# Kernel optimization log

Hardware: AMD Instinct MI355X
Metric: run time of the kernel (lower is better)

The kernel has to match this reference:

```python
import jax, jax.numpy as jnp
import numpy as np

D_MODEL = 512
NHEAD = 8
NUM_LAYERS = 2
INPUT_DIM = 16
DELTA_SCALE = 1.5
LN_EPS = 1e-5


def setup_inputs() -> dict:
    key = jax.random.key(0)
    ks = jax.random.split(key, 16)
    B, S = 16, 1024
    D = D_MODEL
    s_in = 1.0 / np.sqrt(INPUT_DIM)
    s_d = 1.0 / np.sqrt(D)
    return {
        "features": jax.random.normal(ks[0], (B, S, INPUT_DIM), dtype=jnp.float32),
        "hist_w": jax.random.uniform(ks[1], (D, INPUT_DIM), jnp.float32, -s_in, s_in),
        "hist_b": jax.random.uniform(ks[2], (D,), jnp.float32, -s_in, s_in),
        "query_w": jax.random.uniform(ks[3], (D, INPUT_DIM), jnp.float32, -s_in, s_in),
        "query_b": jax.random.uniform(ks[4], (D,), jnp.float32, -s_in, s_in),
        "in_proj_w": jax.random.uniform(ks[5], (NUM_LAYERS, 3 * D, D), jnp.float32, -s_d, s_d),
        "in_proj_b": jnp.zeros((NUM_LAYERS, 3 * D), jnp.float32),
        "attn_out_w": jax.random.uniform(ks[6], (NUM_LAYERS, D, D), jnp.float32, -s_d, s_d),
        "attn_out_b": jnp.zeros((NUM_LAYERS, D), jnp.float32),
        "ln_g": jnp.ones((NUM_LAYERS, D), jnp.float32),
        "ln_b": jnp.zeros((NUM_LAYERS, D), jnp.float32),
        "out_proj_w": jax.random.uniform(ks[7], (1, D), jnp.float32, -s_d, s_d),
        "out_proj_b": jax.random.uniform(ks[8], (1,), jnp.float32, -s_d, s_d),
    }


def _layer_norm(x, g, b):
    mu = jnp.mean(x, axis=-1, keepdims=True)
    var = jnp.var(x, axis=-1, keepdims=True)
    return (x - mu) * jax.lax.rsqrt(var + LN_EPS) * g + b


def _causal_mha(x, kv, wi, bi, wo, bo):
    # x: [B,S,D] queries, kv: [B,S,D] keys/values; query t attends to kv[:t+1]
    B, S, D = x.shape
    hd = D // NHEAD
    wq, wk, wv = wi[:D], wi[D:2 * D], wi[2 * D:]
    bq, bk, bv = bi[:D], bi[D:2 * D], bi[2 * D:]
    q = (x @ wq.T + bq).reshape(B, S, NHEAD, hd)
    k = (kv @ wk.T + bk).reshape(B, S, NHEAD, hd)
    v = (kv @ wv.T + bv).reshape(B, S, NHEAD, hd)
    scale = 1.0 / np.sqrt(hd)
    scores = jnp.einsum('bqhd,bkhd->bhqk', q, k) * scale
    causal = jnp.tril(jnp.ones((S, S), dtype=bool))
    scores = jnp.where(causal, scores, jnp.finfo(scores.dtype).min)
    attn = jax.nn.softmax(scores, axis=-1)
    out = jnp.einsum('bhqk,bkhd->bqhd', attn, v).reshape(B, S, D)
    return out @ wo.T + bo


def reference(features, hist_w, hist_b, query_w, query_b, in_proj_w, in_proj_b,
              attn_out_w, attn_out_b, ln_g, ln_b, out_proj_w, out_proj_b):
    history = features @ hist_w.T + hist_b          # [B,S,D] (fixed K/V)
    x = features @ query_w.T + query_b              # [B,S,D] queries
    for l in range(NUM_LAYERS):
        a = _causal_mha(x, history, in_proj_w[l], in_proj_b[l], attn_out_w[l], attn_out_b[l])
        x = _layer_norm(x + a, ln_g[l], ln_b[l])
    raw = (x @ out_proj_w.T + out_proj_b)[..., 0]   # [B,S]
    return DELTA_SCALE * jnp.tanh(raw)
```

## Files before the change

### kernel.cpp

```cpp
#include <hip/hip_runtime.h>
#include <math.h>

#define DM 512
#define NH 8
#define HD 64
#define BB 16
#define SS 1024
#define NROWS (BB*SS)
#define IND 16
#define KD 512

typedef unsigned short u16;
typedef __attribute__((ext_vector_type(8))) short bf16x8;
typedef __attribute__((ext_vector_type(4))) float f32x4;

static __device__ __forceinline__ u16 f2bf(float f) {
  union { float f; unsigned int u; } v; v.f = f;
  unsigned int r = v.u + 0x7FFFu + ((v.u >> 16) & 1u);
  return (u16)(r >> 16);
}

static __device__ __forceinline__ float dot4(float4 a, float4 b) {
  return a.x*b.x + a.y*b.y + a.z*b.z + a.w*b.w;
}

__global__ __launch_bounds__(256) void k_f2bf_v(const float* __restrict__ in,
                                                u16* __restrict__ out, int n4) {
  int i = blockIdx.x * 256 + threadIdx.x;
  if (i < n4) {
    float4 v = ((const float4*)in)[i];
    ushort4 p;
    p.x = f2bf(v.x); p.y = f2bf(v.y); p.z = f2bf(v.z); p.w = f2bf(v.w);
    ((ushort4*)out)[i] = p;
  }
}

__global__ __launch_bounds__(256) void k_input_proj(
    const float* __restrict__ feat, const float* __restrict__ hw, const float* __restrict__ hb,
    const float* __restrict__ qw, const float* __restrict__ qb,
    u16* __restrict__ histb, float* __restrict__ x, u16* __restrict__ xb) {
  int r0 = blockIdx.x * 16;
  int tid = threadIdx.x;
  int w = tid >> 6, lane = tid & 63;
  __shared__ float f[16][16];
  f[tid >> 4][tid & 15] = feat[(size_t)(r0 + (tid >> 4))*IND + (tid & 15)];
  __syncthreads();

  #pragma unroll
  for (int ch = 0; ch < 2; ch++) {
    int c0 = ch*256 + lane*4;
    {
      float4 wv[4][4];
      #pragma unroll
      for (int j=0;j<4;j++)
        #pragma unroll
        for (int kq=0;kq<4;kq++)
          wv[j][kq] = *(const float4*)(hw + (size_t)(c0+j)*IND + kq*4);
      float b0 = hb[c0], b1 = hb[c0+1], b2 = hb[c0+2], b3 = hb[c0+3];
      #pragma unroll
      for (int rr=0; rr<4; rr++) {
        int row = r0 + w*4 + rr;
        const float4* fr = (const float4*)f[w*4 + rr];
        float4 f0 = fr[0], f1 = fr[1], f2 = fr[2], f3 = fr[3];
        float v0 = b0 + dot4(wv[0][0],f0) + dot4(wv[0][1],f1) + dot4(wv[0][2],f2) + dot4(wv[0][3],f3);
        float v1 = b1 + dot4(wv[1][0],f0) + dot4(wv[1][1],f1) + dot4(wv[1][2],f2) + dot4(wv[1][3],f3);
        float v2 = b2 + dot4(wv[2][0],f0) + dot4(wv[2][1],f1) + dot4(wv[2][2],f2) + dot4(wv[2][3],f3);
        float v3 = b3 + dot4(wv[3][0],f0) + dot4(wv[3][1],f1) + dot4(wv[3][2],f2) + dot4(wv[3][3],f3);
        ushort4 hp; hp.x = f2bf(v0); hp.y = f2bf(v1); hp.z = f2bf(v2); hp.w = f2bf(v3);
        *(ushort4*)&histb[(size_t)row*DM + c0] = hp;
      }
    }
    {
      float4 wv[4][4];
      #pragma unroll
      for (int j=0;j<4;j++)
        #pragma unroll
        for (int kq=0;kq<4;kq++)
          wv[j][kq] = *(const float4*)(qw + (size_t)(c0+j)*IND + kq*4);
      float b0 = qb[c0], b1 = qb[c0+1], b2 = qb[c0+2], b3 = qb[c0+3];
      #pragma unroll
      for (int rr=0; rr<4; rr++) {
        int row = r0 + w*4 + rr;
        const float4* fr = (const float4*)f[w*4 + rr];
        float4 f0 = fr[0], f1 = fr[1], f2 = fr[2], f3 = fr[3];
        float v0 = b0 + dot4(wv[0][0],f0) + dot4(wv[0][1],f1) + dot4(wv[0][2],f2) + dot4(wv[0][3],f3);
        float v1 = b1 + dot4(wv[1][0],f0) + dot4(wv[1][1],f1) + dot4(wv[1][2],f2) + dot4(wv[1][3],f3);
        float v2 = b2 + dot4(wv[2][0],f0) + dot4(wv[2][1],f1) + dot4(wv[2][2],f2) + dot4(wv[2][3],f3);
        float v3 = b3 + dot4(wv[3][0],f0) + dot4(wv[3][1],f1) + dot4(wv[3][2],f2) + dot4(wv[3][3],f3);
        float4 xv; xv.x = v0; xv.y = v1; xv.z = v2; xv.w = v3;
        *(float4*)&x[(size_t)row*DM + c0] = xv;
        ushort4 xp; xp.x = f2bf(v0); xp.y = f2bf(v1); xp.z = f2bf(v2); xp.w = f2bf(v3);
        *(ushort4*)&xb[(size_t)row*DM + c0] = xp;
      }
    }
  }
}

template<int EPI>
__global__ __launch_bounds__(256) void k_bgemm(
    const u16* __restrict__ A, const u16* __restrict__ Wb,
    const float* __restrict__ bias,
    float* __restrict__ Cf, u16* __restrict__ C0h, u16* __restrict__ C1h) {
  __shared__ u16 As[128*64];
  __shared__ u16 Bs[128*64];
  int bm = blockIdx.y * 128, bn = blockIdx.x * 128;
  int tid = threadIdx.x;
  int w = tid >> 6, lane = tid & 63;
  int wm = (w >> 1) * 64, wn = (w & 1) * 64;
  int lq = lane & 15, g = lane >> 4, l7 = lq & 7;

  int srow = tid >> 1;
  int su0 = (tid & 1) * 4;
  const u16* Ag = A  + (size_t)(bm + srow)*KD + su0*8;
  const u16* Bg = Wb + (size_t)(bn + srow)*KD + su0*8;
  int sw[4];
  #pragma unroll
  for (int i=0;i<4;i++) sw[i] = srow*64 + (((su0+i) ^ (srow&7)) << 3);

  f32x4 acc[4][4];
  #pragma unroll
  for (int mf=0;mf<4;mf++)
    #pragma unroll
    for (int nf=0;nf<4;nf++) acc[mf][nf] = (f32x4){0.f,0.f,0.f,0.f};

  #pragma unroll 1
  for (int k0 = 0; k0 < KD; k0 += 64) {
    bf16x8 ar[4], br[4];
    #pragma unroll
    for (int i=0;i<4;i++) {
      ar[i] = *(const bf16x8*)(Ag + k0 + i*8);
      br[i] = *(const bf16x8*)(Bg + k0 + i*8);
    }
    __syncthreads();
    #pragma unroll
    for (int i=0;i<4;i++) { *(bf16x8*)&As[sw[i]] = ar[i]; *(bf16x8*)&Bs[sw[i]] = br[i]; }
    __syncthreads();
    #pragma unroll
    for (int ks=0; ks<2; ks++) {
      int un = ((g + 4*ks) ^ l7) << 3;
      bf16x8 af[4], bfr[4];
      #pragma unroll
      for (int mf=0;mf<4;mf++) af[mf]  = *(const bf16x8*)&As[(wm + mf*16 + lq)*64 + un];
      #pragma unroll
      for (int nf=0;nf<4;nf++) bfr[nf] = *(const bf16x8*)&Bs[(wn + nf*16 + lq)*64 + un];
      #pragma unroll
      for (int mf=0;mf<4;mf++)
        #pragma unroll
        for (int nf=0;nf<4;nf++)
          acc[mf][nf] = __builtin_amdgcn_mfma_f32_16x16x32_bf16(af[mf], bfr[nf], acc[mf][nf], 0, 0, 0);
    }
  }

  float fb[4];
  #pragma unroll
  for (int nf=0;nf<4;nf++) fb[nf] = bias[bn + wn + nf*16 + lq];
  int m0 = bm + wm + g*4;
  int n0 = bn + wn + lq;

  if (EPI == 1 || (EPI == 2 && bn < 512)) {
    const float sc = (EPI == 1) ? 0.125f : 1.0f;
    #pragma unroll
    for (int mf=0;mf<4;mf++) {
      int mb = m0 + mf*16;
      int b = mb >> 10, s = mb & 1023;
      #pragma unroll
      for (int nf=0;nf<4;nf++) {
        int n = n0 + nf*16;
        int h = (n >> 6) & 7, d = n & 63;
        u16* dst = C0h + (((size_t)(b*NH + h))*SS + s)*HD + d;
        #pragma unroll
        for (int r=0;r<4;r++) dst[r*HD] = f2bf((acc[mf][nf][r] + fb[nf]) * sc);
      }
    }
  } else if (EPI == 2) {
    #pragma unroll
    for (int mf=0;mf<4;mf++) {
      int mb = m0 + mf*16;
      int b = mb >> 10, s = mb & 1023;
      #pragma unroll
      for (int nf=0;nf<4;nf++) {
        int n = n0 + nf*16 - 512;
        int h = n >> 6, d = n & 63;
        ushort4 pk;
        pk.x = f2bf(acc[mf][nf][0] + fb[nf]);
        pk.y = f2bf(acc[mf][nf][1] + fb[nf]);
        pk.z = f2bf(acc[mf][nf][2] + fb[nf]);
        pk.w = f2bf(acc[mf][nf][3] + fb[nf]);
        *(ushort4*)&C1h[(((size_t)(b*NH + h))*HD + d)*SS + s] = pk;
      }
    }
  } else {
    #pragma unroll
    for (int mf=0;mf<4;mf++) {
      #pragma unroll
      for (int r=0;r<4;r++) {
        int m = m0 + mf*16 + r;
        #pragma unroll
        for (int nf=0;nf<4;nf++) {
          int n = n0 + nf*16;
          Cf[(size_t)m*DM + n] = acc[mf][nf][r] + fb[nf] + Cf[(size_t)m*DM + n];
        }
      }
    }
  }
}

__global__ __launch_bounds__(512) void k_attn_mfma(
    const u16* __restrict__ Q, const u16* __restrict__ K,
    const u16* __restrict__ Vt, u16* __restrict__ ctxb) {
  int ip = blockIdx.x;
  int bh = blockIdx.y;
  int b = bh >> 3, h = bh & 7;
  int tid = threadIdx.x;
  int w = tid >> 6, lane = tid & 63;
  int lq = lane & 15, g = lane >> 4;
  int l7 = lq & 7;

  __shared__ u16 Ks[4096];
  __shared__ u16 Vs[4096];
  __shared__ u16 Ps[8192];

  int sr = tid >> 3, su = tid & 7;
  int kw = sr*64 + ((su ^ (sr&7)) << 3);
  const u16* kgb = K + ((size_t)bh*SS + sr)*HD + su*8;
  const u16* vgb = Vt + ((size_t)bh*HD + sr)*SS + su*8;
  int pbase = w*1024;

  bf16x8 kreg = *(const bf16x8*)kgb;
  bf16x8 vreg = *(const bf16x8*)vgb;

  #pragma unroll 1
  for (int half = 0; half < 2; half++) {
    int qt2 = half ? (7 - ip) : ip;
    int last = 2*qt2 + 1;

    const u16* qbase = Q + ((size_t)bh*SS + qt2*128 + w*16 + lq)*HD;
    bf16x8 qa0 = *(const bf16x8*)(qbase + g*8);
    bf16x8 qa1 = *(const bf16x8*)(qbase + g*8 + 32);

    f32x4 o[4];
    #pragma unroll
    for (int nb=0;nb<4;nb++) o[nb] = (f32x4){0.f,0.f,0.f,0.f};
    float mrun[4], lrun[4];
    #pragma unroll
    for (int r=0;r<4;r++) { mrun[r] = -1e30f; lrun[r] = 0.f; }

    #pragma unroll 1
    for (int kt = 0; kt <= last; kt++) {
      __syncthreads();
      *(bf16x8*)&Ks[kw] = kreg;
      *(bf16x8*)&Vs[kw] = vreg;
      __syncthreads();
      if (kt < last) {
        kreg = *(const bf16x8*)(kgb + (size_t)(kt+1)*64*HD);
        vreg = *(const bf16x8*)(vgb + (kt+1)*64);
      } else if (half == 0) {
        kreg = *(const bf16x8*)kgb;
        vreg = *(const bf16x8*)vgb;
      }
      if (kt*64 > qt2*128 + w*16 + 15) continue;

      f32x4 s[4];
      #pragma unroll
      for (int nb=0;nb<4;nb++) s[nb] = (f32x4){0.f,0.f,0.f,0.f};
      #pragma unroll
      for (int ks=0; ks<2; ks++) {
        bf16x8 aq = ks ? qa1 : qa0;
        #pragma unroll
        for (int nb=0;nb<4;nb++) {
          bf16x8 kb = *(const bf16x8*)&Ks[(lq + 16*nb)*64 + (((g + 4*ks) ^ l7) << 3)];
          s[nb] = __builtin_amdgcn_mfma_f32_16x16x32_bf16(aq, kb, s[nb], 0, 0, 0);
        }
      }

      bool diag = (kt*64 + 63 > qt2*128 + w*16);
      #pragma unroll
      for (int r=0;r<4;r++) {
        int qrow = qt2*128 + w*16 + g*4 + r;
        if (diag) {
          #pragma unroll
          for (int nb=0;nb<4;nb++)
            if (kt*64 + lq + 16*nb > qrow) s[nb][r] = -1e30f;
        }
        float rm = fmaxf(fmaxf(s[0][r], s[1][r]), fmaxf(s[2][r], s[3][r]));
        #pragma unroll
        for (int off=1; off<16; off<<=1) rm = fmaxf(rm, __shfl_xor(rm, off));
        float mnew = fmaxf(mrun[r], rm);
        float corr = __expf(mrun[r] - mnew);
        float psum = 0.f;
        int mrow = g*4 + r;
        #pragma unroll
        for (int nb=0;nb<4;nb++) {
          float p = __expf(s[nb][r] - mnew);
          psum += p;
          Ps[pbase + mrow*64 + ((((lq>>3) + 2*nb) ^ (mrow&7)) << 3) + l7] = f2bf(p);
        }
        #pragma unroll
        for (int off=1; off<16; off<<=1) psum += __shfl_xor(psum, off);
        lrun[r] = lrun[r]*corr + psum;
        mrun[r] = mnew;
        #pragma unroll
        for (int nb=0;nb<4;nb++) o[nb][r] *= corr;
      }

      #pragma unroll
      for (int ks=0; ks<2; ks++) {
        bf16x8 pa = *(const bf16x8*)&Ps[pbase + lq*64 + (((g + 4*ks) ^ l7) << 3)];
        #pragma unroll
        for (int nb=0;nb<4;nb++) {
          bf16x8 vb = *(const bf16x8*)&Vs[(lq + 16*nb)*64 + (((g + 4*ks) ^ l7) << 3)];
          o[nb] = __builtin_amdgcn_mfma_f32_16x16x32_bf16(pa, vb, o[nb], 0, 0, 0);
        }
      }
    }

    #pragma unroll
    for (int r=0;r<4;r++) {
      float inv = 1.f / lrun[r];
      int qrow = qt2*128 + w*16 + g*4 + r;
      u16* cp = ctxb + ((size_t)b*SS + qrow)*DM + h*HD;
      #pragma unroll
      for (int nb=0;nb<4;nb++) cp[lq + 16*nb] = f2bf(o[nb][r] * inv);
    }
  }
}

__global__ __launch_bounds__(256) void k_ln(
    float* __restrict__ x, const float* __restrict__ g,
    const float* __restrict__ b, u16* __restrict__ xb) {
  int row = blockIdx.x*4 + (threadIdx.x>>6);
  int lane = threadIdx.x & 63;
  float* xr = x + (size_t)row*DM;
  float vals[8]; float s1=0.f, s2=0.f;
  #pragma unroll
  for (int u=0;u<8;u++){ float vv = xr[lane + 64*u]; vals[u]=vv; s1+=vv; s2+=vv*vv; }
  #pragma unroll
  for (int off=1; off<64; off<<=1){ s1 += __shfl_xor(s1,off); s2 += __shfl_xor(s2,off); }
  float mu  = s1 * (1.0f/DM);
  float var = s2 * (1.0f/DM) - mu*mu;
  float inv = rsqrtf(var + 1e-5f);
  u16* xbr = xb + (size_t)row*DM;
  #pragma unroll
  for (int u=0;u<8;u++){
    int c = lane+64*u;
    float vv = (vals[u]-mu)*inv*g[c] + b[c];
    xr[c] = vv;
    xbr[c] = f2bf(vv);
  }
}

__global__ __launch_bounds__(256) void k_head(
    const float* __restrict__ x, const float* __restrict__ w,
    const float* __restrict__ b, float* __restrict__ out) {
  int row = blockIdx.x*4 + (threadIdx.x>>6);
  int lane = threadIdx.x & 63;
  const float* xr = x + (size_t)row*DM;
  float acc = 0.f;
  #pragma unroll
  for (int u=0;u<8;u++) acc += xr[lane+64*u]*w[lane+64*u];
  #pragma unroll
  for (int off=1; off<64; off<<=1) acc += __shfl_xor(acc,off);
  if (lane == 0) out[row] = 1.5f * tanhf(acc + b[0]);
}

extern "C" void kernel_launch(void* const* d_in, const int* in_sizes, int n_in,
                              void* d_out, int out_size, void* d_ws, size_t ws_size,
                              hipStream_t stream) {
  (void)in_sizes; (void)n_in; (void)out_size; (void)ws_size;
  const float* feat      = (const float*)d_in[0];
  const float* hist_w    = (const float*)d_in[1];
  const float* hist_b    = (const float*)d_in[2];
  const float* query_w   = (const float*)d_in[3];
  const float* query_b   = (const float*)d_in[4];
  const float* in_proj_w = (const float*)d_in[5];
  const float* in_proj_b = (const float*)d_in[6];
  const float* attn_w    = (const float*)d_in[7];
  const float* attn_b    = (const float*)d_in[8];
  const float* ln_g      = (const float*)d_in[9];
  const float* ln_b      = (const float*)d_in[10];
  const float* out_w     = (const float*)d_in[11];
  const float* out_b     = (const float*)d_in[12];
  float* out = (float*)d_out;

  float* ws = (float*)d_ws;
  const size_t P = (size_t)NROWS * DM;
  float* x    = ws;
  u16* xb     = (u16*)(ws + P);
  u16* histb  = xb + P;
  u16* ctxb   = histb + P;
  u16* qbf    = ctxb + P;
  u16* kbf    = qbf + P;
  u16* vtb    = kbf + P;
  u16* wipb   = vtb + P;
  u16* wob    = wipb + (size_t)2*3*DM*DM;

  {
    int n4i = 2*3*DM*DM/4, n4o = 2*DM*DM/4;
    k_f2bf_v<<<(n4i+255)/256, 256, 0, stream>>>(in_proj_w, wipb, n4i);
    k_f2bf_v<<<(n4o+255)/256, 256, 0, stream>>>(attn_w, wob, n4o);
  }
  k_input_proj<<<NROWS/16, 256, 0, stream>>>(feat, hist_w, hist_b, query_w, query_b, histb, x, xb);

  for (int l = 0; l < 2; l++) {
    const u16* wq  = wipb + (size_t)l*3*DM*DM;
    const u16* wkv = wq + (size_t)DM*DM;
    const float* bq  = in_proj_b + (size_t)l*3*DM;
    const float* bkv = bq + DM;
    k_bgemm<1><<<dim3(4, 128), 256, 0, stream>>>(xb,    wq,  bq,  nullptr, qbf, nullptr);
    k_bgemm<2><<<dim3(8, 128), 256, 0, stream>>>(histb, wkv, bkv, nullptr, kbf, vtb);
    dim3 ga(4, BB*NH);
    k_attn_mfma<<<ga, 512, 0, stream>>>(qbf, kbf, vtb, ctxb);
    const u16* wo = wob + (size_t)l*DM*DM;
    const float* bo = attn_b + (size_t)l*DM;
    k_bgemm<3><<<dim3(4, 128), 256, 0, stream>>>(ctxb, wo, bo, x, nullptr, nullptr);
    k_ln<<<NROWS/4, 256, 0, stream>>>(x, ln_g + (size_t)l*DM, ln_b + (size_t)l*DM, xb);
  }
  k_head<<<NROWS/4, 256, 0, stream>>>(x, out_w, out_b, out);
}
```

Measured before the change: 422.0 us.

## Double-buffer GEMM tiles with direct global-to-LDS loads

The bf16 GEMM now stages A and B tiles straight from global memory into shared memory using global_load_lds, skipping the register round trip. The shared buffers are doubled so the next K tile is fetched while MFMAs run on the current one, and there is one barrier per iteration instead of two. The XOR swizzle moves into the per-lane global addresses so the LDS layout still matches the fragment reads. This doubles LDS use to 64 KB per block, which may reduce occupancy, and correctness depends on how the builtin orders and waits on its asynchronous writes to LDS.

```diff
diff --git a/kernel.cpp b/kernel.cpp
--- a/kernel.cpp
+++ b/kernel.cpp
@@ -23,6 +23,11 @@
 static __device__ __forceinline__ float dot4(float4 a, float4 b) {
   return a.x*b.x + a.y*b.y + a.z*b.z + a.w*b.w;
 }
+
+#define GLOAD_LDS16(gp, lp)                                                  \
+  __builtin_amdgcn_global_load_lds(                                          \
+      (const __attribute__((address_space(1))) void*)(gp),                   \
+      (__attribute__((address_space(3))) void*)(lp), 16, 0, 0)
 
 __global__ __launch_bounds__(256) void k_f2bf_v(const float* __restrict__ in,
                                                 u16* __restrict__ out, int n4) {
@@ -101,21 +106,18 @@
     const u16* __restrict__ A, const u16* __restrict__ Wb,
     const float* __restrict__ bias,
     float* __restrict__ Cf, u16* __restrict__ C0h, u16* __restrict__ C1h) {
-  __shared__ u16 As[128*64];
-  __shared__ u16 Bs[128*64];
+  __shared__ u16 As[2][128*64];
+  __shared__ u16 Bs[2][128*64];
   int bm = blockIdx.y * 128, bn = blockIdx.x * 128;
   int tid = threadIdx.x;
-  int w = tid >> 6, lane = tid & 63;
-  int wm = (w >> 1) * 64, wn = (w & 1) * 64;
+  int wv = tid >> 6, lane = tid & 63;
+  int wm = (wv >> 1) * 64, wn = (wv & 1) * 64;
   int lq = lane & 15, g = lane >> 4, l7 = lq & 7;
 
-  int srow = tid >> 1;
-  int su0 = (tid & 1) * 4;
-  const u16* Ag = A  + (size_t)(bm + srow)*KD + su0*8;
-  const u16* Bg = Wb + (size_t)(bn + srow)*KD + su0*8;
-  int sw[4];
-  #pragma unroll
-  for (int i=0;i<4;i++) sw[i] = srow*64 + (((su0+i) ^ (srow&7)) << 3);
+  int rsub = lane >> 3;
+  int sug  = (lane & 7) ^ rsub;
+  const u16* Ag = A  + (size_t)(bm + wv*32 + rsub)*KD + sug*8;
+  const u16* Bg = Wb + (size_t)(bn + wv*32 + rsub)*KD + sug*8;
 
   f32x4 acc[4][4];
   #pragma unroll
@@ -123,32 +125,42 @@
     #pragma unroll
     for (int nf=0;nf<4;nf++) acc[mf][nf] = (f32x4){0.f,0.f,0.f,0.f};
 
+  #pragma unroll
+  for (int j=0;j<4;j++) {
+    GLOAD_LDS16(Ag + (size_t)j*8*KD, &As[0][(wv*32 + j*8)*64]);
+    GLOAD_LDS16(Bg + (size_t)j*8*KD, &Bs[0][(wv*32 + j*8)*64]);
+  }
+  __syncthreads();
+
   #pragma unroll 1
-  for (int k0 = 0; k0 < KD; k0 += 64) {
-    bf16x8 ar[4], br[4];
-    #pragma unroll
-    for (int i=0;i<4;i++) {
-      ar[i] = *(const bf16x8*)(Ag + k0 + i*8);
-      br[i] = *(const bf16x8*)(Bg + k0 + i*8);
-    }
-    __syncthreads();
-    #pragma unroll
-    for (int i=0;i<4;i++) { *(bf16x8*)&As[sw[i]] = ar[i]; *(bf16x8*)&Bs[sw[i]] = br[i]; }
-    __syncthreads();
+  for (int t = 0; t < 8; t++) {
+    int cur = t & 1;
+    if (t < 7) {
+      int nxt = cur ^ 1;
+      int k0n = (t+1)*64;
+      #pragma unroll
+      for (int j=0;j<4;j++) {
+        GLOAD_LDS16(Ag + (size_t)j*8*KD + k0n, &As[nxt][(wv*32 + j*8)*64]);
+        GLOAD_LDS16(Bg + (size_t)j*8*KD + k0n, &Bs[nxt][(wv*32 + j*8)*64]);
+      }
+    }
+    const u16* Ac = As[cur];
+    const u16* Bc = Bs[cur];
     #pragma unroll
     for (int ks=0; ks<2; ks++) {
       int un = ((g + 4*ks) ^ l7) << 3;
       bf16x8 af[4], bfr[4];
       #pragma unroll
-      for (int mf=0;mf<4;mf++) af[mf]  = *(const bf16x8*)&As[(wm + mf*16 + lq)*64 + un];
-      #pragma unroll
-      for (int nf=0;nf<4;nf++) bfr[nf] = *(const bf16x8*)&Bs[(wn + nf*16 + lq)*64 + un];
+      for (int mf=0;mf<4;mf++) af[mf]  = *(const bf16x8*)&Ac[(wm + mf*16 + lq)*64 + un];
+      #pragma unroll
+      for (int nf=0;nf<4;nf++) bfr[nf] = *(const bf16x8*)&Bc[(wn + nf*16 + lq)*64 + un];
       #pragma unroll
       for (int mf=0;mf<4;mf++)
         #pragma unroll
         for (int nf=0;nf<4;nf++)
           acc[mf][nf] = __builtin_amdgcn_mfma_f32_16x16x32_bf16(af[mf], bfr[nf], acc[mf][nf], 0, 0, 0);
     }
+    __syncthreads();
   }
 
   float fb[4];
```

New measurement: 412.7 us. 2.2% less time.
